# Optimization experiments

Hardware: AMD Instinct MI355X
Metric: run time of the kernel (lower is better)

The kernel has to match this reference:

```python
import jax, jax.numpy as jnp
import numpy as np

LAYERS = 16
F_SAMPLES = 48   # frequency (pilot subcarrier) samples
T_SAMPLES = 512  # time-domain samples


def dft_matrices(F=F_SAMPLES, T=T_SAMPLES):
    # IDFT: [F, T] maps freq-domain [B,F] -> time-domain [B,T]
    # DFT:  [T, F] maps time-domain [B,T] -> freq-domain [B,F]
    f = np.arange(F)[:, None]
    t = np.arange(T)[None, :]
    ang = 2.0 * np.pi * f * t / T                      # [F, T]
    scale = 1.0 / np.sqrt(T)
    idft_re = jnp.asarray(np.cos(ang) * scale, jnp.float32)   # [F, T]
    idft_im = jnp.asarray(np.sin(ang) * scale, jnp.float32)
    dft_re = jnp.asarray(np.cos(ang).T * scale, jnp.float32)  # [T, F]
    dft_im = jnp.asarray(-np.sin(ang).T * scale, jnp.float32)
    return dft_re, dft_im, idft_re, idft_im


def mm(a_re, a_im, b_re, b_im):
    # complex matmul (a_re + i a_im) @ (b_re + i b_im) via 4 real GEMMs
    return (a_re @ b_re - a_im @ b_im,
            a_re @ b_im + a_im @ b_re)


def soft_gate(x, s1, s2):
    # sigmoid(x, S1, S2) = logistic(S1 * (x - S2)) -- soft-threshold gate
    return jax.nn.sigmoid(s1 * (x - s2))


def setup_inputs() -> dict:
    key = jax.random.key(0)
    u = jax.random.normal(key, (16384, F_SAMPLES, 2), dtype=jnp.float32)
    S1 = jnp.full((1,), 10.0, dtype=jnp.float32)
    S2 = jnp.full((1,), 0.5, dtype=jnp.float32)
    return {"u": u, "S1": S1, "S2": S2}


def reference(u, S1, S2):
    dft_re, dft_im, idft_re, idft_im = dft_matrices()
    B = u.shape[0]

    maximum = jnp.abs(u.max())
    u = 5.0 * u / maximum
    u_re, u_im = u[:, :, 0], u[:, :, 1]

    z_re, z_im = u_re, u_im
    H_re = jnp.zeros((B, T_SAMPLES), jnp.float32)
    H_im = jnp.zeros((B, T_SAMPLES), jnp.float32)

    def layer(carry, _):
        z_re, z_im, H_re, H_im = carry
        Z_re, Z_im = mm(z_re, z_im, idft_re, idft_im)      # [B, T]
        R_re = H_re + Z_re
        R_im = H_im + Z_im
        R_mean = jnp.sqrt(jnp.mean(R_re * R_re + R_im * R_im, axis=0))  # [T]
        g = soft_gate(R_mean, S1[0], S2[0])                # [T]
        H_re = R_re * g
        H_im = R_im * g
        h_re, h_im = mm(H_re, H_im, dft_re, dft_im)        # [B, F]
        z_re = u_re - h_re
        z_im = u_im - h_im
        return (z_re, z_im, H_re, H_im), None

    (z_re, z_im, H_re, H_im), _ = jax.lax.scan(
        layer, (z_re, z_im, H_re, H_im), None, length=LAYERS)

    h_re, h_im = mm(H_re, H_im, dft_re, dft_im)            # [B, F]
    out = jnp.stack((h_re, h_im), axis=2)                  # [B, F, 2]
    out = out / 5.0 * maximum
    return out
```

## Files before the change

kernel.cpp:

```cpp
#include <hip/hip_runtime.h>
#include <math.h>

#define NROWS 16384
#define FC 96
#define T 512
#define NRI 1024
#define NPAIR 512
#define LAYERS 16
#define NBLK 256

typedef _Float16 f16;
typedef _Float16 half8 __attribute__((ext_vector_type(8)));
typedef _Float16 half4 __attribute__((ext_vector_type(4)));
typedef float floatx4 __attribute__((ext_vector_type(4)));
typedef float floatx2 __attribute__((ext_vector_type(2)));

#define OFF_MAXKEY 0
#define OFF_ARR  64
#define OFF_REL  (OFF_ARR + NBLK * 32)
#define OFF_W1   (OFF_REL + NBLK * 32)
#define OFF_W1L  (OFF_W1 + 49152)
#define OFF_W2   (OFF_W1L + 49152)
#define OFF_W2L  (OFF_W2 + 49152)
#define OFF_PART (OFF_W2L + 49152)
#define OFF_FIN  (OFF_PART + NPAIR * NBLK)

#define SMEM_BYTES 157696

__global__ void ksetup(float* __restrict__ ws) {
    int t = threadIdx.x;
    if (t == 0)
        __hip_atomic_store((unsigned*)(ws + OFF_MAXKEY), 0u, __ATOMIC_RELAXED, __HIP_MEMORY_SCOPE_AGENT);
    for (int i = t; i < 2 * NBLK * 32; i += 256)
        __hip_atomic_store((unsigned*)(ws + OFF_ARR) + i, 0u, __ATOMIC_RELAXED, __HIP_MEMORY_SCOPE_AGENT);
}

__global__ void kwf(float* __restrict__ ws) {
    int idx = blockIdx.x * 256 + threadIdx.x;
    if (idx >= 2 * 98304) return;
    int which = idx >= 98304;
    int id = which ? idx - 98304 : idx;
    int j = id & 7, lane = (id >> 3) & 63, rem = id >> 9;
    int k, n;
    if (!which) { int kc = rem % 3,  nt = rem / 3;  k = kc*32 + (lane>>4)*8 + j; n = nt*16 + (lane&15); }
    else        { int kc = rem & 31, nt = rem >> 5; k = kc*32 + (lane>>4)*8 + j; n = nt*16 + (lane&15); }
    int t, f, q, e;
    if (!which) { t = n >> 1; e = n & 1; f = k >> 1; q = k & 1; }
    else        { t = k >> 1; q = k & 1; f = n >> 1; e = n & 1; }
    int ft = (f * t) & (T - 1);
    float sv, cv;
    sincosf((float)ft * 0.012271846303085129f, &sv, &cv);
    const float sc = 0.04419417382415922f;
    cv *= sc; sv *= sc;
    float val;
    if (!which) val = (e == 0) ? (q == 0 ? cv : -sv) : (q == 0 ?  sv : cv);
    else        val = (e == 0) ? (q == 0 ? cv :  sv) : (q == 0 ? -sv : cv);
    f16 hi = (f16)val;
    f16 lo = (f16)(val - (float)hi);
    f16* H = (f16*)(ws + (which ? OFF_W2 : OFF_W1));
    f16* L = (f16*)(ws + (which ? OFF_W2L : OFF_W1L));
    H[id] = hi;
    L[id] = lo;
}

__device__ __forceinline__ void gbar2(float* __restrict__ ws, unsigned e) {
    asm volatile("s_waitcnt vmcnt(0)" ::: "memory");
    __syncthreads();
    const int tid = threadIdx.x;
    unsigned* __restrict__ Af = (unsigned*)(ws + OFF_ARR);
    unsigned* __restrict__ Rf = (unsigned*)(ws + OFF_REL);
    if (blockIdx.x == 0) {
        if (tid < 64) {
            bool ok;
            do {
                __builtin_amdgcn_s_sleep(1);
                ok = true;
#pragma unroll
                for (int s = 0; s < NBLK / 64; s++) {
                    int b = s * 64 + tid;
                    unsigned v = __hip_atomic_load(&Af[b * 32], __ATOMIC_RELAXED, __HIP_MEMORY_SCOPE_AGENT);
                    ok = ok && (b == 0 || v >= e);
                }
            } while (!__all(ok));
            asm volatile("" ::: "memory");
#pragma unroll
            for (int s = 0; s < NBLK / 64; s++) {
                int b = s * 64 + tid;
                __hip_atomic_store(&Rf[b * 32], e, __ATOMIC_RELAXED, __HIP_MEMORY_SCOPE_AGENT);
            }
        }
        __syncthreads();
    } else {
        if (tid == 0) {
            __hip_atomic_store(&Af[blockIdx.x * 32], e, __ATOMIC_RELAXED, __HIP_MEMORY_SCOPE_AGENT);
            while (__hip_atomic_load(&Rf[blockIdx.x * 32], __ATOMIC_RELAXED, __HIP_MEMORY_SCOPE_AGENT) < e)
                __builtin_amdgcn_s_sleep(2);
            asm volatile("" ::: "memory");
        }
        __syncthreads();
    }
}

__device__ __forceinline__ void coh_store4(float* p, float v) {
    asm volatile("global_store_dword %0, %1, off sc0 sc1" :: "v"(p), "v"(v) : "memory");
}
__device__ __forceinline__ void coh_store8v(float* p, floatx2 v) {
    asm volatile("global_store_dwordx2 %0, %1, off sc0 sc1" :: "v"(p), "v"(v) : "memory");
}
__device__ __forceinline__ void coh_load2x16(const float* pa, const float* pb,
                                             floatx4& va, floatx4& vb) {
    asm volatile("global_load_dwordx4 %0, %2, off sc0 sc1\n\t"
                 "global_load_dwordx4 %1, %3, off sc0 sc1\n\t"
                 "s_waitcnt vmcnt(0)"
                 : "=&v"(va), "=&v"(vb)
                 : "v"(pa), "v"(pb)
                 : "memory");
}

__global__ __launch_bounds__(512, 2) void kmain(const float* __restrict__ u,
                                                const float* __restrict__ S1,
                                                const float* __restrict__ S2,
                                                float* __restrict__ out,
                                                float* __restrict__ ws) {
    extern __shared__ char smem[];
    f16* zh = (f16*)smem;
    f16* zl = zh + 64 * FC;
    f16* Hs = zl + 64 * FC;
    float* garr = (float*)(Hs + 64 * NRI);
    __shared__ float smax[8];

    const int tid = threadIdx.x;
    const int w = tid >> 6;
    const int lane = tid & 63;
    const int q = lane >> 4;
    const int l15 = lane & 15;
    const int row0 = blockIdx.x * 64;
    const float s1 = S1[0], s2 = S2[0];

    unsigned epoch = 1;

    float m = -1e30f;
    for (int i = tid; i < 64 * FC; i += 512) m = fmaxf(m, u[(long)row0 * FC + i]);
#pragma unroll
    for (int s = 1; s < 64; s <<= 1) m = fmaxf(m, __shfl_xor(m, s, 64));
    if (lane == 0) smax[w] = m;
    __syncthreads();
    if (tid == 0) {
        float mm = smax[0];
#pragma unroll
        for (int i = 1; i < 8; i++) mm = fmaxf(mm, smax[i]);
        unsigned k = __float_as_uint(mm);
        k = (k & 0x80000000u) ? ~k : (k | 0x80000000u);
        atomicMax((unsigned*)(ws + OFF_MAXKEY), k);
    }
    gbar2(ws, epoch); epoch++;
    unsigned key = __hip_atomic_load((unsigned*)(ws + OFF_MAXKEY), __ATOMIC_RELAXED, __HIP_MEMORY_SCOPE_AGENT);
    unsigned ku = (key & 0x80000000u) ? (key ^ 0x80000000u) : ~key;
    const float gmax = fabsf(__uint_as_float(ku));
    const float sc_to = 5.0f / gmax;
    const float sc_from = gmax / 5.0f;

    for (int i = tid; i < 64 * FC; i += 512) {
        int b = i / FC, fc = i - b * FC;
        float z = sc_to * u[(long)row0 * FC + i];
        f16 h = (f16)z;
        int idx = b * FC + ((fc & ~31) | ((fc & 31) ^ ((b & 3) << 3)));
        zh[idx] = h;
        zl[idx] = (f16)(z - (float)h);
    }

    floatx4 R[32];
#pragma unroll
    for (int i = 0; i < 32; i++) R[i] = (floatx4){0.f, 0.f, 0.f, 0.f};

    const f16* __restrict__ w1h = (const f16*)(ws + OFF_W1);
    const f16* __restrict__ w1l = (const f16*)(ws + OFF_W1L);
    const f16* __restrict__ w2h = (const f16*)(ws + OFF_W2);
    const f16* __restrict__ w2l = (const f16*)(ws + OFF_W2L);
    float* __restrict__ partP = ws + OFF_PART;
    float* __restrict__ fin = ws + OFF_FIN;

    const int brow = (w & 3) * 16 + l15;
    const int fh = (w >> 2) * 3;
    const int aswz = (brow & 7) << 3;
    const long hrow = (long)brow * NRI;

    float gcur = 0.0f;

#pragma unroll 1
    for (int l = 0; l < LAYERS; l++) {
        __syncthreads();

        if (l > 0) {
#pragma unroll
            for (int ntl = 0; ntl < 8; ntl++) {
                float ga = __shfl(gcur, ntl * 8 + q * 2, 64);
                float gb = __shfl(gcur, ntl * 8 + q * 2 + 1, 64);
#pragma unroll
                for (int bt = 0; bt < 4; bt++) {
                    R[ntl * 4 + bt][0] *= ga;
                    R[ntl * 4 + bt][1] *= ga;
                    R[ntl * 4 + bt][2] *= gb;
                    R[ntl * 4 + bt][3] *= gb;
                }
            }
        }
#pragma unroll
        for (int kc = 0; kc < 3; kc++) {
            half8 Bh[4], Bl[4];
#pragma unroll
            for (int bt = 0; bt < 4; bt++) {
                int b = bt * 16 + l15;
                int zi = b * FC + kc * 32 + ((q ^ (b & 3)) << 3);
                Bh[bt] = *(const half8*)(zh + zi);
                Bl[bt] = *(const half8*)(zl + zi);
            }
#pragma unroll
            for (int ntl = 0; ntl < 8; ntl++) {
                int wi = (((w * 8 + ntl) * 3 + kc) * 64 + lane) * 8;
                half8 Ah = *(const half8*)(w1h + wi);
                half8 Al = *(const half8*)(w1l + wi);
#pragma unroll
                for (int bt = 0; bt < 4; bt++) {
                    R[ntl*4+bt] = __builtin_amdgcn_mfma_f32_16x16x32_f16(Ah, Bh[bt], R[ntl*4+bt], 0, 0, 0);
                    R[ntl*4+bt] = __builtin_amdgcn_mfma_f32_16x16x32_f16(Ah, Bl[bt], R[ntl*4+bt], 0, 0, 0);
                    R[ntl*4+bt] = __builtin_amdgcn_mfma_f32_16x16x32_f16(Al, Bh[bt], R[ntl*4+bt], 0, 0, 0);
                }
            }
        }

#pragma unroll
        for (int ntl = 0; ntl < 8; ntl++) {
            floatx4 ps;
#pragma unroll
            for (int r = 0; r < 4; r++) {
                float p = R[ntl*4+0][r] * R[ntl*4+0][r];
                p = fmaf(R[ntl*4+1][r], R[ntl*4+1][r], p);
                p = fmaf(R[ntl*4+2][r], R[ntl*4+2][r], p);
                p = fmaf(R[ntl*4+3][r], R[ntl*4+3][r], p);
                p += __shfl_xor(p, 1, 64);
                p += __shfl_xor(p, 2, 64);
                p += __shfl_xor(p, 4, 64);
                p += __shfl_xor(p, 8, 64);
                ps[r] = p;
            }
            if (l15 == 0) {
                int p0 = w * 64 + ntl * 8 + q * 2;
                coh_store4(partP + p0 * NBLK + blockIdx.x, ps[0] + ps[1]);
                coh_store4(partP + (p0 + 1) * NBLK + blockIdx.x, ps[2] + ps[3]);
            }
        }
        gbar2(ws, epoch); epoch++;

        if (w == 0) {
            const float* pa = partP + (2 * blockIdx.x) * NBLK + 4 * lane;
            const float* pb = partP + (2 * blockIdx.x + 1) * NBLK + 4 * lane;
            floatx4 va, vb;
            coh_load2x16(pa, pb, va, vb);
            float c0 = va[0] + va[1] + va[2] + va[3];
            float c1 = vb[0] + vb[1] + vb[2] + vb[3];
#pragma unroll
            for (int sh = 1; sh < 64; sh <<= 1) {
                c0 += __shfl_xor(c0, sh, 64);
                c1 += __shfl_xor(c1, sh, 64);
            }
            if (lane == 0) coh_store8v(fin + 2 * blockIdx.x, (floatx2){c0, c1});
        }
        gbar2(ws, epoch); epoch++;

        if (w == 0) {
            floatx4 va, vb;
            coh_load2x16(fin + 4 * lane, fin + 256 + 4 * lane, va, vb);
            *(floatx4*)(garr + 4 * lane) = va;
            *(floatx4*)(garr + 256 + 4 * lane) = vb;
        }
        __syncthreads();
        {
            float sum = garr[w * 64 + lane];
            float rm = sqrtf(sum * (1.0f / 16384.0f));
            gcur = 1.0f / (1.0f + expf(-s1 * (rm - s2)));
        }

#pragma unroll
        for (int ntl = 0; ntl < 8; ntl++) {
            float ga = __shfl(gcur, ntl * 8 + q * 2, 64);
            float gb = __shfl(gcur, ntl * 8 + q * 2 + 1, 64);
            floatx4 g4 = {ga, ga, gb, gb};
            int col = w * 128 + ntl * 16 + q * 4;
#pragma unroll
            for (int bt = 0; bt < 4; bt++) {
                int row = bt * 16 + l15;
                half4 vh;
#pragma unroll
                for (int r = 0; r < 4; r++) vh[r] = (f16)(g4[r] * R[ntl * 4 + bt][r]);
                *(half4*)(Hs + row * NRI + (col ^ ((row & 7) << 3))) = vh;
            }
        }
        __syncthreads();

        floatx4 acc[3];
#pragma unroll
        for (int i = 0; i < 3; i++) acc[i] = (floatx4){0.f, 0.f, 0.f, 0.f};
#pragma unroll 4
        for (int kg = 0; kg < 32; kg++) {
            half8 Ah = *(const half8*)(Hs + hrow + ((kg * 32 + q * 8) ^ aswz));
#pragma unroll
            for (int ft = 0; ft < 3; ft++) {
                int wi = (((fh + ft) * 32 + kg) * 64 + lane) * 8;
                half8 Wh = *(const half8*)(w2h + wi);
                half8 Wl = *(const half8*)(w2l + wi);
                acc[ft] = __builtin_amdgcn_mfma_f32_16x16x32_f16(Ah, Wh, acc[ft], 0, 0, 0);
                acc[ft] = __builtin_amdgcn_mfma_f32_16x16x32_f16(Ah, Wl, acc[ft], 0, 0, 0);
            }
        }

        if (l < LAYERS - 1) {
#pragma unroll
            for (int ft = 0; ft < 3; ft++) {
                int fcg = (fh + ft) * 16 + l15;
#pragma unroll
                for (int r = 0; r < 4; r++) {
                    int b = (w & 3) * 16 + q * 4 + r;
                    float z = fmaf(sc_to, u[(long)(row0 + b) * FC + fcg], -acc[ft][r]);
                    f16 h = (f16)z;
                    int idx = b * FC + ((fcg & ~31) | ((fcg & 31) ^ ((b & 3) << 3)));
                    zh[idx] = h;
                    zl[idx] = (f16)(z - (float)h);
                }
            }
        } else {
#pragma unroll
            for (int ft = 0; ft < 3; ft++) {
                int fcg = (fh + ft) * 16 + l15;
#pragma unroll
                for (int r = 0; r < 4; r++) {
                    int b = (w & 3) * 16 + q * 4 + r;
                    out[(long)(row0 + b) * FC + fcg] = acc[ft][r] * sc_from;
                }
            }
        }
    }
}

extern "C" void kernel_launch(void* const* d_in, const int* in_sizes, int n_in,
                              void* d_out, int out_size, void* d_ws, size_t ws_size,
                              hipStream_t stream) {
    (void)in_sizes; (void)n_in; (void)out_size; (void)ws_size;
    const float* u  = (const float*)d_in[0];
    const float* S1 = (const float*)d_in[1];
    const float* S2 = (const float*)d_in[2];
    float* out = (float*)d_out;
    float* ws  = (float*)d_ws;

    static int inited = 0;
    if (!inited) {
        hipFuncSetAttribute((const void*)kmain, hipFuncAttributeMaxDynamicSharedMemorySize, SMEM_BYTES);
        inited = 1;
    }

    ksetup<<<1, 256, 0, stream>>>(ws);
    kwf<<<768, 256, 0, stream>>>(ws);

    void* args[] = {(void*)&u, (void*)&S1, (void*)&S2, (void*)&out, (void*)&ws};
    hipLaunchCooperativeKernel((const void*)kmain, dim3(NBLK), dim3(512), args,
                               (unsigned)SMEM_BYTES, stream);
}
```

Baseline: 1.297 ms.

## Drop split-fp16 compensation GEMMs, transpose partial-sum layout, alternate barrier master

Removes the hi/lo fp16 error-compensation terms, so the IDFT GEMM uses one MFMA instead of three and the DFT GEMM one instead of two. The low-part LDS buffer and weight loads go away, which cuts shared memory use. The per-block partial sums are now stored contiguously per block as 8-byte coherent stores and read back with strided 64-bit atomic loads, and the grid-barrier master block alternates between two blocks by epoch. The cost is lower precision: the matmuls now run in plain fp16 with fp32 accumulation across 16 layers, which may break the accuracy tolerance.

```diff
diff --git a/kernel.cpp b/kernel.cpp
--- a/kernel.cpp
+++ b/kernel.cpp
@@ -23,9 +23,9 @@
 #define OFF_W2   (OFF_W1L + 49152)
 #define OFF_W2L  (OFF_W2 + 49152)
 #define OFF_PART (OFF_W2L + 49152)
-#define OFF_FIN  (OFF_PART + NPAIR * NBLK)
-
-#define SMEM_BYTES 157696
+#define OFF_FIN  (OFF_PART + NBLK * NPAIR)
+
+#define SMEM_BYTES 145408
 
 __global__ void ksetup(float* __restrict__ ws) {
     int t = threadIdx.x;
@@ -67,9 +67,10 @@
     asm volatile("s_waitcnt vmcnt(0)" ::: "memory");
     __syncthreads();
     const int tid = threadIdx.x;
+    const unsigned swb = (e & 1u) ? (NBLK / 2) : 0;
     unsigned* __restrict__ Af = (unsigned*)(ws + OFF_ARR);
     unsigned* __restrict__ Rf = (unsigned*)(ws + OFF_REL);
-    if (blockIdx.x == 0) {
+    if (blockIdx.x == swb) {
         if (tid < 64) {
             bool ok;
             do {
@@ -77,15 +78,15 @@
                 ok = true;
 #pragma unroll
                 for (int s = 0; s < NBLK / 64; s++) {
-                    int b = s * 64 + tid;
+                    unsigned b = s * 64 + tid;
                     unsigned v = __hip_atomic_load(&Af[b * 32], __ATOMIC_RELAXED, __HIP_MEMORY_SCOPE_AGENT);
-                    ok = ok && (b == 0 || v >= e);
+                    ok = ok && (b == swb || v >= e);
                 }
             } while (!__all(ok));
             asm volatile("" ::: "memory");
 #pragma unroll
             for (int s = 0; s < NBLK / 64; s++) {
-                int b = s * 64 + tid;
+                unsigned b = s * 64 + tid;
                 __hip_atomic_store(&Rf[b * 32], e, __ATOMIC_RELAXED, __HIP_MEMORY_SCOPE_AGENT);
             }
         }
@@ -101,9 +102,6 @@
     }
 }
 
-__device__ __forceinline__ void coh_store4(float* p, float v) {
-    asm volatile("global_store_dword %0, %1, off sc0 sc1" :: "v"(p), "v"(v) : "memory");
-}
 __device__ __forceinline__ void coh_store8v(float* p, floatx2 v) {
     asm volatile("global_store_dwordx2 %0, %1, off sc0 sc1" :: "v"(p), "v"(v) : "memory");
 }
@@ -124,8 +122,7 @@
                                                 float* __restrict__ ws) {
     extern __shared__ char smem[];
     f16* zh = (f16*)smem;
-    f16* zl = zh + 64 * FC;
-    f16* Hs = zl + 64 * FC;
+    f16* Hs = zh + 64 * FC;
     float* garr = (float*)(Hs + 64 * NRI);
     __shared__ float smax[8];
 
@@ -163,10 +160,8 @@
     for (int i = tid; i < 64 * FC; i += 512) {
         int b = i / FC, fc = i - b * FC;
         float z = sc_to * u[(long)row0 * FC + i];
-        f16 h = (f16)z;
         int idx = b * FC + ((fc & ~31) | ((fc & 31) ^ ((b & 3) << 3)));
-        zh[idx] = h;
-        zl[idx] = (f16)(z - (float)h);
+        zh[idx] = (f16)z;
     }
 
     floatx4 R[32];
@@ -174,9 +169,7 @@
     for (int i = 0; i < 32; i++) R[i] = (floatx4){0.f, 0.f, 0.f, 0.f};
 
     const f16* __restrict__ w1h = (const f16*)(ws + OFF_W1);
-    const f16* __restrict__ w1l = (const f16*)(ws + OFF_W1L);
     const f16* __restrict__ w2h = (const f16*)(ws + OFF_W2);
-    const f16* __restrict__ w2l = (const f16*)(ws + OFF_W2L);
     float* __restrict__ partP = ws + OFF_PART;
     float* __restrict__ fin = ws + OFF_FIN;
 
@@ -207,72 +200,74 @@
         }
 #pragma unroll
         for (int kc = 0; kc < 3; kc++) {
-            half8 Bh[4], Bl[4];
+            half8 Bh[4];
 #pragma unroll
             for (int bt = 0; bt < 4; bt++) {
                 int b = bt * 16 + l15;
                 int zi = b * FC + kc * 32 + ((q ^ (b & 3)) << 3);
                 Bh[bt] = *(const half8*)(zh + zi);
-                Bl[bt] = *(const half8*)(zl + zi);
             }
 #pragma unroll
             for (int ntl = 0; ntl < 8; ntl++) {
                 int wi = (((w * 8 + ntl) * 3 + kc) * 64 + lane) * 8;
                 half8 Ah = *(const half8*)(w1h + wi);
-                half8 Al = *(const half8*)(w1l + wi);
 #pragma unroll
                 for (int bt = 0; bt < 4; bt++) {
                     R[ntl*4+bt] = __builtin_amdgcn_mfma_f32_16x16x32_f16(Ah, Bh[bt], R[ntl*4+bt], 0, 0, 0);
-                    R[ntl*4+bt] = __builtin_amdgcn_mfma_f32_16x16x32_f16(Ah, Bl[bt], R[ntl*4+bt], 0, 0, 0);
-                    R[ntl*4+bt] = __builtin_amdgcn_mfma_f32_16x16x32_f16(Al, Bh[bt], R[ntl*4+bt], 0, 0, 0);
-                }
-            }
-        }
-
-#pragma unroll
-        for (int ntl = 0; ntl < 8; ntl++) {
-            floatx4 ps;
-#pragma unroll
-            for (int r = 0; r < 4; r++) {
-                float p = R[ntl*4+0][r] * R[ntl*4+0][r];
-                p = fmaf(R[ntl*4+1][r], R[ntl*4+1][r], p);
-                p = fmaf(R[ntl*4+2][r], R[ntl*4+2][r], p);
-                p = fmaf(R[ntl*4+3][r], R[ntl*4+3][r], p);
-                p += __shfl_xor(p, 1, 64);
-                p += __shfl_xor(p, 2, 64);
-                p += __shfl_xor(p, 4, 64);
-                p += __shfl_xor(p, 8, 64);
-                ps[r] = p;
-            }
-            if (l15 == 0) {
-                int p0 = w * 64 + ntl * 8 + q * 2;
-                coh_store4(partP + p0 * NBLK + blockIdx.x, ps[0] + ps[1]);
-                coh_store4(partP + (p0 + 1) * NBLK + blockIdx.x, ps[2] + ps[3]);
+                }
+            }
+        }
+
+        {
+            float* part = partP + (long)blockIdx.x * NPAIR;
+#pragma unroll
+            for (int ntl = 0; ntl < 8; ntl++) {
+                floatx4 ps;
+#pragma unroll
+                for (int r = 0; r < 4; r++) {
+                    float p = R[ntl*4+0][r] * R[ntl*4+0][r];
+                    p = fmaf(R[ntl*4+1][r], R[ntl*4+1][r], p);
+                    p = fmaf(R[ntl*4+2][r], R[ntl*4+2][r], p);
+                    p = fmaf(R[ntl*4+3][r], R[ntl*4+3][r], p);
+                    p += __shfl_xor(p, 1, 64);
+                    p += __shfl_xor(p, 2, 64);
+                    p += __shfl_xor(p, 4, 64);
+                    p += __shfl_xor(p, 8, 64);
+                    ps[r] = p;
+                }
+                if (l15 == 0) {
+                    int pr = w * 64 + ntl * 8 + q * 2;
+                    coh_store8v(part + pr, (floatx2){ps[0] + ps[1], ps[2] + ps[3]});
+                }
             }
         }
         gbar2(ws, epoch); epoch++;
 
         if (w == 0) {
-            const float* pa = partP + (2 * blockIdx.x) * NBLK + 4 * lane;
-            const float* pb = partP + (2 * blockIdx.x + 1) * NBLK + 4 * lane;
-            floatx4 va, vb;
-            coh_load2x16(pa, pb, va, vb);
-            float c0 = va[0] + va[1] + va[2] + va[3];
-            float c1 = vb[0] + vb[1] + vb[2] + vb[3];
+            const int p0 = blockIdx.x * 2;
+            float c0 = 0.f, c1 = 0.f;
+#pragma unroll
+            for (int s4 = 0; s4 < 4; s4++) {
+                unsigned long long a = __hip_atomic_load(
+                    (const unsigned long long*)(partP + (long)(s4 * 64 + lane) * NPAIR + p0),
+                    __ATOMIC_RELAXED, __HIP_MEMORY_SCOPE_AGENT);
+                c0 += __uint_as_float((unsigned)a);
+                c1 += __uint_as_float((unsigned)(a >> 32));
+            }
 #pragma unroll
             for (int sh = 1; sh < 64; sh <<= 1) {
                 c0 += __shfl_xor(c0, sh, 64);
                 c1 += __shfl_xor(c1, sh, 64);
             }
-            if (lane == 0) coh_store8v(fin + 2 * blockIdx.x, (floatx2){c0, c1});
+            if (lane == 0) coh_store8v(fin + p0, (floatx2){c0, c1});
         }
         gbar2(ws, epoch); epoch++;
 
         if (w == 0) {
             floatx4 va, vb;
-            coh_load2x16(fin + 4 * lane, fin + 256 + 4 * lane, va, vb);
-            *(floatx4*)(garr + 4 * lane) = va;
-            *(floatx4*)(garr + 256 + 4 * lane) = vb;
+            coh_load2x16(fin + 8 * lane, fin + 8 * lane + 4, va, vb);
+            *(floatx4*)(garr + 8 * lane) = va;
+            *(floatx4*)(garr + 8 * lane + 4) = vb;
         }
         __syncthreads();
         {
@@ -308,9 +303,7 @@
             for (int ft = 0; ft < 3; ft++) {
                 int wi = (((fh + ft) * 32 + kg) * 64 + lane) * 8;
                 half8 Wh = *(const half8*)(w2h + wi);
-                half8 Wl = *(const half8*)(w2l + wi);
                 acc[ft] = __builtin_amdgcn_mfma_f32_16x16x32_f16(Ah, Wh, acc[ft], 0, 0, 0);
-                acc[ft] = __builtin_amdgcn_mfma_f32_16x16x32_f16(Ah, Wl, acc[ft], 0, 0, 0);
             }
         }
 
@@ -322,10 +315,8 @@
                 for (int r = 0; r < 4; r++) {
                     int b = (w & 3) * 16 + q * 4 + r;
                     float z = fmaf(sc_to, u[(long)(row0 + b) * FC + fcg], -acc[ft][r]);
-                    f16 h = (f16)z;
                     int idx = b * FC + ((fcg & ~31) | ((fcg & 31) ^ ((b & 3) << 3)));
-                    zh[idx] = h;
-                    zl[idx] = (f16)(z - (float)h);
+                    zh[idx] = (f16)z;
                 }
             }
         } else {
```

New measurement: 1.160 ms. -10.6%, faster.
